# Kernel tuning notes

Hardware: AMD Instinct MI355X
Metric: run time of the kernel (lower is better)

Reference implementation:

```python
import jax, jax.numpy as jnp
import numpy as np

N, D = 65536, 256


def _unit(x):
    # contrastive embeddings are L2-normalized; also keeps exp(dot) finite
    return x / jnp.linalg.norm(x, axis=-1, keepdims=True)


def setup_inputs() -> dict:
    key = jax.random.key(0)
    k1, k2 = jax.random.split(key)
    z_a = _unit(jax.random.normal(k1, (N, D), dtype=jnp.float32))
    z_b = _unit(jax.random.normal(k2, (N, D), dtype=jnp.float32))
    return {"z_a": z_a, "z_b": z_b}


def reference(z_a, z_b):
    # d_i = dot(z_a[i], z_b[i])  (the only quantity the original ever computes)
    n = z_a.shape[0]
    d = jnp.sum(z_a * z_b, axis=-1)  # [n]
    # Original loop structure:
    #   alignment      = sum_i (-d_i)
    #   negative_sum_i = (# of j in range(n-1), j != i) * d_i
    #                  = (n-2) * d_i for i < n-1, (n-1) * d_i for i == n-1
    #   uniformity_i   = exp(d_i)
    counts = jnp.full((n,), n - 2, dtype=d.dtype).at[n - 1].set(n - 1)
    return jnp.sum((counts - 1.0) * d + jnp.exp(d))
```

## Files before the change

kernel.cpp:

```cpp
#include <hip/hip_runtime.h>
#include <math.h>


#define D_DIM 256
#define ROWS_PER_WAVE 8
#define WAVES_PER_BLOCK 4

typedef __attribute__((address_space(1))) const unsigned int gu32_t;
typedef __attribute__((address_space(3))) unsigned int su32_t;

__device__ __forceinline__ void gload_lds16(const void* g, void* l) {
    __builtin_amdgcn_global_load_lds((gu32_t*)g, (su32_t*)l, 16, 0, 0);
}

__global__ __launch_bounds__(256, 2)
void dot_loss_partial(const float4* __restrict__ za4,
                      const float4* __restrict__ zb4,
                      float* __restrict__ partial,
                      int n) {
    __shared__ __align__(16) float A[WAVES_PER_BLOCK][ROWS_PER_WAVE][D_DIM];
    __shared__ __align__(16) float B[WAVES_PER_BLOCK][ROWS_PER_WAVE][D_DIM];

    const int lane = threadIdx.x & 63;
    const int wave = threadIdx.x >> 6;
    const int row0 = (blockIdx.x * WAVES_PER_BLOCK + wave) * ROWS_PER_WAVE;

    const float4* a = za4 + (size_t)row0 * 64 + lane;
    const float4* b = zb4 + (size_t)row0 * 64 + lane;

    #pragma unroll
    for (int r = 0; r < ROWS_PER_WAVE; ++r) {
        gload_lds16(a + (size_t)r * 64, &A[wave][r][0]);
        gload_lds16(b + (size_t)r * 64, &B[wave][r][0]);
    }
    __builtin_amdgcn_s_waitcnt(0);
    __builtin_amdgcn_sched_barrier(0);

    const int rowIdx = lane & 7;
    const int cj = lane >> 3;
    const float4* Ar = reinterpret_cast<const float4*>(&A[wave][rowIdx][0]);
    const float4* Br = reinterpret_cast<const float4*>(&B[wave][rowIdx][0]);
    float s = 0.0f;
    #pragma unroll
    for (int c = 0; c < 8; ++c) {
        const int f = cj * 8 + ((c + rowIdx) & 7);
        float4 av = Ar[f];
        float4 bv = Br[f];
        s = fmaf(av.x, bv.x, s);
        s = fmaf(av.y, bv.y, s);
        s = fmaf(av.z, bv.z, s);
        s = fmaf(av.w, bv.w, s);
    }
    s += __shfl_down(s, 32);
    s += __shfl_down(s, 16);
    s += __shfl_down(s, 8);

    float acc = 0.0f;
    if (lane < 8) {
        const int row = row0 + lane;
        const float coeff = (row == n - 1) ? (float)(n - 2) : (float)(n - 3);
        acc = coeff * s + expf(s);
    }
    acc += __shfl_down(acc, 4);
    acc += __shfl_down(acc, 2);
    acc += __shfl_down(acc, 1);

    __shared__ float smem[WAVES_PER_BLOCK];
    if (lane == 0) smem[wave] = acc;
    __syncthreads();
    if (threadIdx.x == 0) {
        float s2 = 0.0f;
        #pragma unroll
        for (int w = 0; w < WAVES_PER_BLOCK; ++w) s2 += smem[w];
        partial[blockIdx.x] = s2;
    }
}

__global__ __launch_bounds__(256)
void reduce_partials(const float* __restrict__ partial,
                     float* __restrict__ out,
                     int m) {
    const int lane = threadIdx.x & 63;
    const int wave = threadIdx.x >> 6;
    double s = 0.0;
    for (int i = threadIdx.x; i < m; i += 256)
        s += (double)partial[i];
    #pragma unroll
    for (int off = 32; off > 0; off >>= 1)
        s += __shfl_down(s, off);
    __shared__ double smem[4];
    if (lane == 0) smem[wave] = s;
    __syncthreads();
    if (threadIdx.x == 0)
        out[0] = (float)(smem[0] + smem[1] + smem[2] + smem[3]);
}

extern "C" void kernel_launch(void* const* d_in, const int* in_sizes, int n_in,
                              void* d_out, int out_size, void* d_ws, size_t ws_size,
                              hipStream_t stream) {
    const float4* za4 = (const float4*)d_in[0];
    const float4* zb4 = (const float4*)d_in[1];
    float* out = (float*)d_out;
    float* partial = (float*)d_ws;
    const int n = in_sizes[0] / D_DIM;
    const int blocks = n / (ROWS_PER_WAVE * WAVES_PER_BLOCK);

    dot_loss_partial<<<blocks, 256, 0, stream>>>(za4, zb4, partial, n);
    reduce_partials<<<1, 256, 0, stream>>>(partial, out, blocks);
}
```

Baseline: 145.4 us.

## Double-buffer per-wave row chunks to overlap global loads with dot products

```diff
diff --git a/kernel.cpp b/kernel.cpp
--- a/kernel.cpp
+++ b/kernel.cpp
@@ -3,7 +3,9 @@
 
 
 #define D_DIM 256
-#define ROWS_PER_WAVE 8
+#define ROWS_PER_CHUNK 4
+#define CHUNKS_PER_WAVE 8
+#define ROWS_PER_WAVE (ROWS_PER_CHUNK * CHUNKS_PER_WAVE)
 #define WAVES_PER_BLOCK 4
 
 typedef __attribute__((address_space(1))) const unsigned int gu32_t;
@@ -18,8 +20,8 @@
                       const float4* __restrict__ zb4,
                       float* __restrict__ partial,
                       int n) {
-    __shared__ __align__(16) float A[WAVES_PER_BLOCK][ROWS_PER_WAVE][D_DIM];
-    __shared__ __align__(16) float B[WAVES_PER_BLOCK][ROWS_PER_WAVE][D_DIM];
+    __shared__ __align__(16) float SA[WAVES_PER_BLOCK][2][ROWS_PER_CHUNK][D_DIM];
+    __shared__ __align__(16) float SB[WAVES_PER_BLOCK][2][ROWS_PER_CHUNK][D_DIM];
 
     const int lane = threadIdx.x & 63;
     const int wave = threadIdx.x >> 6;
@@ -28,40 +30,58 @@
     const float4* a = za4 + (size_t)row0 * 64 + lane;
     const float4* b = zb4 + (size_t)row0 * 64 + lane;
 
-    #pragma unroll
-    for (int r = 0; r < ROWS_PER_WAVE; ++r) {
-        gload_lds16(a + (size_t)r * 64, &A[wave][r][0]);
-        gload_lds16(b + (size_t)r * 64, &B[wave][r][0]);
-    }
-    __builtin_amdgcn_s_waitcnt(0);
-    __builtin_amdgcn_sched_barrier(0);
-
-    const int rowIdx = lane & 7;
-    const int cj = lane >> 3;
-    const float4* Ar = reinterpret_cast<const float4*>(&A[wave][rowIdx][0]);
-    const float4* Br = reinterpret_cast<const float4*>(&B[wave][rowIdx][0]);
-    float s = 0.0f;
-    #pragma unroll
-    for (int c = 0; c < 8; ++c) {
-        const int f = cj * 8 + ((c + rowIdx) & 7);
-        float4 av = Ar[f];
-        float4 bv = Br[f];
-        s = fmaf(av.x, bv.x, s);
-        s = fmaf(av.y, bv.y, s);
-        s = fmaf(av.z, bv.z, s);
-        s = fmaf(av.w, bv.w, s);
-    }
-    s += __shfl_down(s, 32);
-    s += __shfl_down(s, 16);
-    s += __shfl_down(s, 8);
+    const int r_ = lane & 3;
+    const int q_ = lane >> 2;
 
     float acc = 0.0f;
-    if (lane < 8) {
-        const int row = row0 + lane;
-        const float coeff = (row == n - 1) ? (float)(n - 2) : (float)(n - 3);
-        acc = coeff * s + expf(s);
+
+    #pragma unroll
+    for (int r = 0; r < ROWS_PER_CHUNK; ++r) {
+        gload_lds16(a + (size_t)r * 64, &SA[wave][0][r][0]);
+        gload_lds16(b + (size_t)r * 64, &SB[wave][0][r][0]);
     }
-    acc += __shfl_down(acc, 4);
+
+    #pragma unroll
+    for (int c = 0; c < CHUNKS_PER_WAVE; ++c) {
+        const int cur = c & 1;
+        if (c + 1 < CHUNKS_PER_WAVE) {
+            const int nxt = cur ^ 1;
+            #pragma unroll
+            for (int r = 0; r < ROWS_PER_CHUNK; ++r) {
+                const size_t gr = (size_t)((c + 1) * ROWS_PER_CHUNK + r) * 64;
+                gload_lds16(a + gr, &SA[wave][nxt][r][0]);
+                gload_lds16(b + gr, &SB[wave][nxt][r][0]);
+            }
+            asm volatile("s_waitcnt vmcnt(8)" ::: "memory");
+        } else {
+            asm volatile("s_waitcnt vmcnt(0)" ::: "memory");
+        }
+        __builtin_amdgcn_sched_barrier(0);
+
+        const float4* Ar = reinterpret_cast<const float4*>(&SA[wave][cur][r_][0]);
+        const float4* Br = reinterpret_cast<const float4*>(&SB[wave][cur][r_][0]);
+        float s = 0.0f;
+        #pragma unroll
+        for (int t = 0; t < 4; ++t) {
+            const int f = q_ * 4 + ((t + r_) & 3);
+            float4 av = Ar[f];
+            float4 bv = Br[f];
+            s = fmaf(av.x, bv.x, s);
+            s = fmaf(av.y, bv.y, s);
+            s = fmaf(av.z, bv.z, s);
+            s = fmaf(av.w, bv.w, s);
+        }
+        s += __shfl_down(s, 32);
+        s += __shfl_down(s, 16);
+        s += __shfl_down(s, 8);
+        s += __shfl_down(s, 4);
+        if (lane < 4) {
+            const int row = row0 + c * ROWS_PER_CHUNK + lane;
+            const float coeff = (row == n - 1) ? (float)(n - 2) : (float)(n - 3);
+            acc += coeff * s + expf(s);
+        }
+    }
+
     acc += __shfl_down(acc, 2);
     acc += __shfl_down(acc, 1);
 
```

Measured after the change: 142.7 us. About the same (-1.9%).
